# Optimization experiments

Measured on AMD Instinct MI355X. Metric: run time of the kernel, lower is better.

## Reference

```python
import jax, jax.numpy as jnp
import numpy as np

EPS = 1e-10
BETA = 1.0  # beta passed to VectorQuantizer in Encoder_conv


def _conv(x, w, b, stride, pad):
    # x: NCHW, w: OIHW
    y = jax.lax.conv_general_dilated(x, w, window_strides=stride, padding=pad,
                                     dimension_numbers=('NCHW', 'OIHW', 'NCHW'))
    if b is not None:
        y = y + b[None, :, None, None]
    return y


def _forward(x, w_in, b_in, w_h1, b_h1, w_h2, b_h2, w_h3, b_h3,
             r0_w1, r0_w2, r1_w1, r1_w2, emb):
    relu = jax.nn.relu
    h = relu(_conv(x, w_in, b_in, (2, 2), [(1, 1), (1, 1)]))      # [B,128,256,256]
    h = relu(_conv(h, w_h1, b_h1, (4, 4), [(2, 2), (2, 2)]))      # [B,256,64,64]
    h = relu(_conv(h, w_h2, b_h2, (4, 4), [(2, 2), (2, 2)]))      # [B,256,16,16]
    h = relu(_conv(h, w_h3, b_h3, (2, 2), [(1, 1), (1, 1)]))      # [B,256,8,8]
    # ResidualBlock with 2 Residual layers: relu->conv[1,3]->relu->conv[1,1], no bias
    for wa, wb in ((r0_w1, r0_w2), (r1_w1, r1_w2)):
        t = _conv(relu(h), wa, None, (1, 1), [(0, 0), (1, 1)])
        t = _conv(relu(t), wb, None, (1, 1), [(0, 0), (0, 0)])
        h = h + t
    h = relu(h)
    # VectorQuantizer
    lat = jnp.transpose(h, (0, 2, 3, 1))                          # [B,H,W,D]
    D = emb.shape[1]
    flat = lat.reshape(-1, D)                                     # [N,D]
    dist = (jnp.sum(flat * flat, axis=1, keepdims=True)
            + jnp.sum(emb * emb, axis=1)
            - 2.0 * flat @ emb.T)                                 # [N,K]
    idx = jnp.argmin(dist, axis=1)                                # [N]
    quant = emb[idx].reshape(lat.shape)                           # [B,H,W,D]
    sg = jax.lax.stop_gradient
    e_loss = jnp.mean((sg(quant) - lat) ** 2)
    q_loss = jnp.mean((quant - sg(lat)) ** 2)
    loss = q_loss + BETA * e_loss
    quant_st = lat + sg(quant - lat)                              # straight-through
    probs = jnp.mean(jax.nn.one_hot(idx, emb.shape[0], dtype=lat.dtype), axis=0)
    perplexity = jnp.exp(-jnp.sum(probs * jnp.log(probs + EPS)))
    return jnp.transpose(quant_st, (0, 3, 1, 2)), loss, perplexity


def setup_inputs() -> dict:
    key = jax.random.key(0)
    ks = jax.random.split(key, 14)
    C_in, C, K = 3, 256, 512
    s = 0.05
    f32 = jnp.float32
    return {
        'x':     jax.random.normal(ks[0], (8, C_in, 512, 512), f32),
        'w_in':  jax.random.normal(ks[1], (C // 2, C_in, 4, 4), f32) * s,
        'b_in':  jnp.zeros((C // 2,), f32),
        'w_h1':  jax.random.normal(ks[2], (C, C // 2, 7, 7), f32) * s,
        'b_h1':  jnp.zeros((C,), f32),
        'w_h2':  jax.random.normal(ks[3], (C, C, 7, 7), f32) * s,
        'b_h2':  jnp.zeros((C,), f32),
        'w_h3':  jax.random.normal(ks[4], (C, C, 3, 3), f32) * s,
        'b_h3':  jnp.zeros((C,), f32),
        'r0_w1': jax.random.normal(ks[5], (4 * C, C, 1, 3), f32) * s,
        'r0_w2': jax.random.normal(ks[6], (C, 4 * C, 1, 1), f32) * s,
        'r1_w1': jax.random.normal(ks[7], (4 * C, C, 1, 3), f32) * s,
        'r1_w2': jax.random.normal(ks[8], (C, 4 * C, 1, 1), f32) * s,
        'emb':   jax.random.uniform(ks[9], (K, C), f32, -1.0 / K, 1.0 / K),
    }


def reference(x, w_in, b_in, w_h1, b_h1, w_h2, b_h2, w_h3, b_h3,
              r0_w1, r0_w2, r1_w1, r1_w2, emb):
    return _forward(x, w_in, b_in, w_h1, b_h1, w_h2, b_h2, w_h3, b_h3,
                    r0_w1, r0_w2, r1_w1, r1_w2, emb)
```

## Files before the change

### kernel.cpp

```cpp
#include <hip/hip_runtime.h>
#include <hip/hip_bf16.h>

typedef __hip_bfloat16 bf16;
typedef __attribute__((ext_vector_type(4))) float f32x4;
typedef __attribute__((ext_vector_type(8))) short short8;

__device__ __forceinline__ float b2f(bf16 v) { return __bfloat162float(v); }
__device__ __forceinline__ ushort f2bu(float v)
{
    bf16 b = __float2bfloat16(v);
    return *(ushort*)&b;
}
__device__ __forceinline__ uint relu2(uint v)
{
    uint r = v;
    if (r & 0x8000u)     r &= 0xFFFF0000u;
    if (r & 0x80000000u) r &= 0x0000FFFFu;
    return r;
}
__device__ __forceinline__ uint packbf2(float a, float b)
{
    uint lo = f2bu(a), hi = f2bu(b);
    return lo | (hi << 16);
}

typedef const __attribute__((address_space(1))) unsigned int* as1_u32;
typedef __attribute__((address_space(3))) unsigned int* as3_u32;
__device__ __forceinline__ void gld16(const void* g, uint* l)
{
    __builtin_amdgcn_global_load_lds((as1_u32)g, (as3_u32)l, 16, 0, 0);
}

__global__ __launch_bounds__(256) void initw_k(
        const float* __restrict__ w_in, const float* __restrict__ w_h1,
        const float* __restrict__ w_h2, const float* __restrict__ w_h3,
        const float* __restrict__ r0w1, const float* __restrict__ r0w2,
        const float* __restrict__ r1w1, const float* __restrict__ r1w2,
        const float* __restrict__ emb,
        bf16* __restrict__ wp1, bf16* __restrict__ wpack2, bf16* __restrict__ wpack3,
        bf16* __restrict__ wp4, bf16* __restrict__ wpA0, bf16* __restrict__ wpA1,
        bf16* __restrict__ wpB0, bf16* __restrict__ wpB1,
        float* __restrict__ en, float* __restrict__ mse, int* __restrict__ hist,
        float* __restrict__ zpad)
{
    __shared__ ushort ls[12544];
    int b = blockIdx.x, t = threadIdx.x;

    if (b < 256) {
        const float* src = w_h1 + (size_t)b * 6272;
        for (int i = t; i < 6272; i += 256) ls[i] = f2bu(src[i]);
        __syncthreads();
        for (int e = t; e < 800; e += 256) {
            int tap = e >> 4, cib8 = e & 15;
            short8 v;
            #pragma unroll
            for (int cil = 0; cil < 8; ++cil)
                v[cil] = (tap < 49) ? (short)ls[(cib8 * 8 + cil) * 49 + tap] : (short)0;
            *(short8*)(wpack2 + ((size_t)(tap * 16 + cib8) * 256 + b) * 8) = v;
        }
        return;
    }
    if (b < 512) {
        int co = b - 256;
        const float* src = w_h2 + (size_t)co * 12544;
        for (int i = t; i < 12544; i += 256) ls[i] = f2bu(src[i]);
        __syncthreads();
        for (int e = t; e < 1600; e += 256) {
            int tap = e >> 5, cib8 = e & 31;
            short8 v;
            #pragma unroll
            for (int cil = 0; cil < 8; ++cil)
                v[cil] = (tap < 49) ? (short)ls[(cib8 * 8 + cil) * 49 + tap] : (short)0;
            *(short8*)(wpack3 + ((size_t)(tap * 32 + cib8) * 256 + co) * 8) = v;
        }
        return;
    }
    if (b < 768) {
        int co = b - 512;
        const float* src = w_h3 + (size_t)co * 2304;
        for (int i = t; i < 2304; i += 256) ls[i] = f2bu(src[i]);
        __syncthreads();
        for (int e = t; e < 288; e += 256) {
            int tap = e >> 5, cib8 = e & 31;
            short8 v;
            #pragma unroll
            for (int cil = 0; cil < 8; ++cil)
                v[cil] = (short)ls[(cib8 * 8 + cil) * 9 + tap];
            *(short8*)(wp4 + ((size_t)(tap * 32 + cib8) * 256 + co) * 8) = v;
        }
        return;
    }
    if (b < 2816) {
        int r = b - 768;
        int which = r >> 10;
        int co = r & 1023;
        const float* srcb = which ? r1w1 : r0w1;
        bf16* dstb = which ? wpA1 : wpA0;
        const float* src = srcb + (size_t)co * 768;
        for (int i = t; i < 768; i += 256) ls[i] = f2bu(src[i]);
        __syncthreads();
        if (t < 96) {
            int tap = t >> 5, cib8 = t & 31;
            short8 v;
            #pragma unroll
            for (int cil = 0; cil < 8; ++cil)
                v[cil] = (short)ls[(cib8 * 8 + cil) * 3 + tap];
            *(short8*)(dstb + ((size_t)(tap * 32 + cib8) * 1024 + co) * 8) = v;
        }
        return;
    }
    if (b < 3072) {
        int r = b - 2816;
        int which = r >> 7;
        const float* srcb = which ? r1w2 : r0w2;
        bf16* dstb = which ? wpB1 : wpB0;
        int c = (r & 127) * 256 + t;
        int cib8 = c >> 8, co = c & 255;
        const float* s = srcb + (size_t)co * 1024 + cib8 * 8;
        short8 v;
        #pragma unroll
        for (int cil = 0; cil < 8; ++cil) v[cil] = (short)f2bu(s[cil]);
        *(short8*)(dstb + (size_t)c * 8) = v;
        return;
    }
    if (b < 3104) {
        int i = (b - 3072) * 256 + t;
        int j = i & 7; int co = (i >> 3) & 127; int kb = i >> 10;
        int k = kb * 8 + j;
        wp1[i] = __float2bfloat16(k < 48 ? w_in[co * 48 + k] : 0.f);
        return;
    }
    if (b < 3106) {
        int row = (b - 3104) * 256 + t;
        const float4* e = (const float4*)(emb + (size_t)row * 256);
        float s = 0.f;
        for (int d4 = 0; d4 < 64; ++d4) {
            float4 v = e[d4];
            s += v.x * v.x + v.y * v.y + v.z * v.z + v.w * v.w;
        }
        en[row] = s;
        return;
    }
    if (t == 0) mse[0] = 0.f;
    for (int i = t; i < 512; i += 256) hist[i] = 0;
    if (t < 64) zpad[t] = 0.f;
}

__global__ __launch_bounds__(256) void conv1m_k(const float* __restrict__ x,
        const bf16* __restrict__ wp1, const float* __restrict__ bias,
        bf16* __restrict__ h1c)
{
    int bid = blockIdx.x;
    int pxt = bid & 511, img = bid >> 9;
    int tr = pxt >> 4, tc = pxt & 15;
    int oh0 = tr * 8, ow0 = tc * 16;
    const float* xi = x + (size_t)img * 786432;
    bf16* oT = h1c + (size_t)img * 8388608;

    int t = threadIdx.x;
    int wave = t >> 6, lane = t & 63;
    int quad = lane >> 4, l15 = lane & 15;

    __shared__ ushort xs[4 * 640];
    __shared__ ushort ot[128 * 136];

    int ihb = oh0 * 2 - 1, iwb = ow0 * 2 - 1;
    for (int i = t; i < 1836; i += 256) {
        int ci = i / 612; int r1 = i - ci * 612;
        int ihl = r1 / 34, iwl = r1 - ihl * 34;
        int ih = ihb + ihl, iw = iwb + iwl;
        float v = 0.f;
        if ((unsigned)ih < 512u && (unsigned)iw < 512u)
            v = xi[ci * 262144 + ih * 512 + iw];
        xs[ci * 640 + ihl * 35 + iwl] = f2bu(v);
    }
    for (int i = t; i < 640; i += 256) xs[3 * 640 + i] = 0;
    __syncthreads();

    f32x4 zero = {0.f, 0.f, 0.f, 0.f};
    f32x4 acc[8][2];
    #pragma unroll
    for (int m = 0; m < 8; ++m) { acc[m][0] = zero; acc[m][1] = zero; }

    int ci_b = quad >> 1;
    int kh0 = (quad & 1) * 2;
    int iwl0 = 2 * l15;

    #pragma unroll
    for (int ks = 0; ks < 2; ++ks) {
        union { short8 v; uint u[4]; } b[2];
        #pragma unroll
        for (int nt = 0; nt < 2; ++nt) {
            int py = wave * 2 + nt;
            int base = (ks * 2 + ci_b) * 640 + (2 * py + kh0) * 35 + iwl0;
            b[nt].u[0] = *(const uint*)&xs[base];
            b[nt].u[1] = *(const uint*)&xs[base + 2];
            b[nt].u[2] = *(const uint*)&xs[base + 35];
            b[nt].u[3] = *(const uint*)&xs[base + 37];
        }
        const bf16* abase = wp1 + ((size_t)(ks * 4 + quad) * 128 + l15) * 8;
        #pragma unroll
        for (int m = 0; m < 8; ++m) {
            short8 a = *(const short8*)(abase + m * 16 * 8);
            acc[m][0] = __builtin_amdgcn_mfma_f32_16x16x32_bf16(a, b[0].v, acc[m][0], 0, 0, 0);
            acc[m][1] = __builtin_amdgcn_mfma_f32_16x16x32_bf16(a, b[1].v, acc[m][1], 0, 0, 0);
        }
    }

    #pragma unroll
    for (int m = 0; m < 8; ++m) {
        int cobase = m * 16 + quad * 4;
        float b0 = bias[cobase], b1 = bias[cobase + 1];
        float b2 = bias[cobase + 2], b3 = bias[cobase + 3];
        #pragma unroll
        for (int nt = 0; nt < 2; ++nt) {
            int pxl = (wave * 2 + nt) * 16 + l15;
            uint w0 = packbf2(fmaxf(b0 + acc[m][nt][0], 0.f),
                              fmaxf(b1 + acc[m][nt][1], 0.f));
            uint w1 = packbf2(fmaxf(b2 + acc[m][nt][2], 0.f),
                              fmaxf(b3 + acc[m][nt][3], 0.f));
            *(uint*)&ot[pxl * 136 + cobase]     = w0;
            *(uint*)&ot[pxl * 136 + cobase + 2] = w1;
        }
    }
    __syncthreads();
    {
        int pxl = t >> 1, half = t & 1;
        int oh = oh0 + (pxl >> 4), ow = ow0 + (pxl & 15);
        size_t px = (size_t)(oh * 256 + ow);
        #pragma unroll
        for (int cb = 0; cb < 4; ++cb) {
            int c16 = half * 4 + cb;
            const uint4* src = (const uint4*)&ot[pxl * 136 + c16 * 16];
            uint4* dst = (uint4*)(oT + ((size_t)c16 * 65536 + px) * 16);
            dst[0] = src[0];
            dst[1] = src[1];
        }
    }
}

template <int IH, int OH, int CI, int SPLIT, int MODE>
__global__ __launch_bounds__(256, 2) void conv_mfma9_k(
        const bf16* __restrict__ inC, const bf16* __restrict__ wpack,
        const float* __restrict__ bias, float* __restrict__ outA,
        bf16* __restrict__ outT, const float* __restrict__ zpad)
{
    constexpr int TPD = OH / 8;
    constexpr int NT = TPD * TPD;
    constexpr int CPB = (CI / 16) / SPLIT;
    constexpr int CIB8 = CI / 8;
    constexpr int NPX = IH * IH;
    constexpr int SLOTS = 2496;

    int bid = blockIdx.x;
    int pxt = bid % NT;
    int rest = bid / NT;
    int img = rest & 7;
    int split = rest >> 3;
    int oh0 = (pxt / TPD) * 8, ow0 = (pxt % TPD) * 8;

    int t = threadIdx.x;
    int wave = t >> 6, lane = t & 63;
    int quad = lane >> 4, l15 = lane & 15;

    const bf16* inb = inC + (size_t)img * ((size_t)NPX * CI);

    __shared__ __align__(16) uint bufA[SLOTS * 4];
    __shared__ __align__(16) uint bufB[SLOTS * 4];

    f32x4 zero = {0.f, 0.f, 0.f, 0.f};
    f32x4 acc[4][4];
    #pragma unroll
    for (int a = 0; a < 4; ++a)
        #pragma unroll
        for (int b = 0; b < 4; ++b) acc[a][b] = zero;

    int ihb = oh0 * 4 - 2, iwb = ow0 * 4 - 2;
    int qxl = l15 & 7, pyl = l15 >> 3;
    int tap_par = quad >> 1, ci_half = quad & 1;

    int  srel[10];
    bool sval[10];
    #pragma unroll
    for (int it = 0; it < 10; ++it) {
        int sb = (it < 9) ? it * 256 + wave * 64 : 2304 + wave * 64;
        int p  = sb + lane;
        int pb = p << 4;
        int lb = pb ^ (((pb >> 7) & 7) << 4);
        int j  = lb >> 4;
        int pos = j >> 1, half = j & 1;
        int r = pos / 35, c = pos - r * 35;
        int ih = ihb + r, iw = iwb + c;
        sval[it] = (j < 2450) && ((unsigned)ih < (unsigned)IH)
                   && ((unsigned)iw < (unsigned)IH);
        srel[it] = (ih * IH + iw) * 16 + half * 8;
    }

    auto stage = [&](int ch, uint* dst) {
        const bf16* cbp = inb + (size_t)ch * NPX * 16;
        #pragma unroll
        for (int it = 0; it < 10; ++it) {
            if (it == 9 && wave >= 3) continue;
            int sb = (it < 9) ? it * 256 + wave * 64 : 2304 + wave * 64;
            const void* src = sval[it] ? (const void*)(cbp + srel[it])
                                       : (const void*)zpad;
            gld16(src, dst + sb * 4);
        }
    };

    int rbase = pyl * 4480 + qxl * 128 + ci_half * 16;
    int d1  = tap_par * 32;
    int d29 = tap_par * 928;

    auto compute = [&](int ch, const uint* cbuf) {
        const bf16* ab = wpack
            + ((size_t)(ch * 2 + ci_half) * 256 + wave * 64 + l15) * 8
            + (size_t)tap_par * (CIB8 * 2048);
        __builtin_amdgcn_s_setprio(1);
        short8 aC[4], bC[4], aN[4], bN[4];
        {
            #pragma unroll
            for (int ct = 0; ct < 4; ++ct)
                aC[ct] = *(const short8*)(ab + ct * 128);
            int lbb = rbase + d1;
            #pragma unroll
            for (int pt = 0; pt < 4; ++pt) {
                int lb = lbb + pt * 8960;
                int pb = lb ^ (((lb >> 7) & 7) << 4);
                bC[pt] = *(const short8*)((const char*)cbuf + pb);
            }
        }
        #pragma unroll
        for (int tp = 0; tp < 25; ++tp) {
            if (tp < 24) {
                const int tn  = tp + 1;
                const int kh0 = (2 * tn) / 7, kw0 = (2 * tn) % 7;
                const int cE  = (kh0 * 35 + kw0) * 32;
                int dsel = (tn == 24) ? 0 : ((kw0 == 6) ? d29 : d1);
                int lbb  = rbase + cE + dsel;
                const bf16* at = ab + (size_t)(2 * tn) * (CIB8 * 2048);
                #pragma unroll
                for (int ct = 0; ct < 4; ++ct)
                    aN[ct] = *(const short8*)(at + ct * 128);
                #pragma unroll
                for (int pt = 0; pt < 4; ++pt) {
                    int lb = lbb + pt * 8960;
                    int pb = lb ^ (((lb >> 7) & 7) << 4);
                    bN[pt] = *(const short8*)((const char*)cbuf + pb);
                }
            }
            #pragma unroll
            for (int pt = 0; pt < 4; ++pt)
                #pragma unroll
                for (int ct = 0; ct < 4; ++ct)
                    acc[ct][pt] = __builtin_amdgcn_mfma_f32_16x16x32_bf16(
                        aC[ct], bC[pt], acc[ct][pt], 0, 0, 0);
            if (tp < 24) {
                #pragma unroll
                for (int i = 0; i < 4; ++i) { aC[i] = aN[i]; bC[i] = bN[i]; }
            }
        }
        __builtin_amdgcn_s_setprio(0);
    };

    if constexpr (CPB == 1) {
        stage(split, bufA);
        __syncthreads();
        compute(split, bufA);
    } else {
        stage(split * CPB, bufA);
        __syncthreads();
        for (int cc2 = 0; cc2 < CPB; cc2 += 2) {
            stage(split * CPB + cc2 + 1, bufB);
            compute(split * CPB + cc2, bufA);
            __syncthreads();
            if (cc2 + 2 < CPB) stage(split * CPB + cc2 + 2, bufA);
            compute(split * CPB + cc2 + 1, bufB);
            __syncthreads();
        }
    }

    #pragma unroll
    for (int ct = 0; ct < 4; ++ct) {
        int cobase = wave * 64 + ct * 16 + quad * 4;
        #pragma unroll
        for (int pt = 0; pt < 4; ++pt) {
            int px = pt * 16 + l15;
            int oh = oh0 + (px >> 3), ow = ow0 + (px & 7);
            int pxg = oh * OH + ow;
            if (MODE == 3) {
                #pragma unroll
                for (int r = 0; r < 4; ++r) {
                    int co = cobase + r;
                    outA[(size_t)split * ((size_t)8 * OH * OH * 256)
                         + (size_t)img * (OH * OH * 256)
                         + (size_t)co * (OH * OH) + pxg] = acc[ct][pt][r];
                }
            } else {
                float o0 = fmaxf(bias[cobase]     + acc[ct][pt][0], 0.f);
                float o1 = fmaxf(bias[cobase + 1] + acc[ct][pt][1], 0.f);
                float o2 = fmaxf(bias[cobase + 2] + acc[ct][pt][2], 0.f);
                float o3 = fmaxf(bias[cobase + 3] + acc[ct][pt][3], 0.f);
                uint2 w;
                w.x = packbf2(o0, o1);
                w.y = packbf2(o2, o3);
                size_t base = (size_t)img * (size_t)(OH * OH * 256);
                *(uint2*)(outT + base
                          + ((size_t)(wave * 4 + ct) * (OH * OH) + pxg) * 16
                          + quad * 4) = w;
            }
        }
    }
}

__global__ void combine3_k(const float* __restrict__ p3, const float* __restrict__ bias,
                           bf16* __restrict__ h3T)
{
    int idx = blockIdx.x * 256 + threadIdx.x;
    int px = idx & 255;
    int co = (idx >> 8) & 255;
    int img = idx >> 16;
    float v = bias[co];
    #pragma unroll
    for (int s = 0; s < 8; ++s) v += p3[(size_t)s * 524288 + idx];
    v = fmaxf(v, 0.f);
    h3T[((size_t)img * 256 + px) * 256 + co] = __float2bfloat16(v);
}

__global__ __launch_bounds__(256) void conv4m_k(const bf16* __restrict__ h3T,
        const bf16* __restrict__ wp4, const float* __restrict__ bias,
        bf16* __restrict__ h4T)
{
    int bid = blockIdx.x;
    int img = bid >> 2, cog = bid & 3;
    int t = threadIdx.x;
    int wave = t >> 6, lane = t & 63;
    int quad = lane >> 4, l15 = lane & 15;

    __shared__ uint pt[16 * 325];

    for (int i = t; i < 16 * 325; i += 256) pt[i] = 0;

    f32x4 zero = {0.f, 0.f, 0.f, 0.f};
    f32x4 acc[4];
    #pragma unroll
    for (int b = 0; b < 4; ++b) acc[b] = zero;

    const bf16* inb = h3T + (size_t)img * 65536;

    for (int ch = 0; ch < 8; ++ch) {
        __syncthreads();
        for (int e = t; e < 4096; e += 256) {
            int cp = e & 15, px = e >> 4;
            int py = px >> 4, qx = px & 15;
            uint v = *(const uint*)(inb + (size_t)px * 256 + ch * 32 + cp * 2);
            pt[cp * 325 + (py + 1) * 18 + qx + 1] = v;
        }
        __syncthreads();

        for (int tap = 0; tap < 9; ++tap) {
            int kh = tap / 3, kw = tap - kh * 3;
            const bf16* abase = wp4 + ((size_t)((tap * 32 + ch * 4 + quad) * 256)
                                       + cog * 64 + wave * 16 + l15) * 8;
            short8 a = *(const short8*)abase;
            #pragma unroll
            for (int pq = 0; pq < 4; ++pq) {
                int pyo = 2 * pq + (l15 >> 3);
                int ipos = (2 * pyo + kh) * 18 + 2 * (l15 & 7) + kw;
                union { short8 v; uint u[4]; } b;
                b.u[0] = pt[(quad * 4 + 0) * 325 + ipos];
                b.u[1] = pt[(quad * 4 + 1) * 325 + ipos];
                b.u[2] = pt[(quad * 4 + 2) * 325 + ipos];
                b.u[3] = pt[(quad * 4 + 3) * 325 + ipos];
                acc[pq] = __builtin_amdgcn_mfma_f32_16x16x32_bf16(
                    a, b.v, acc[pq], 0, 0, 0);
            }
        }
    }

    int cobase = cog * 64 + wave * 16 + quad * 4;
    #pragma unroll
    for (int pq = 0; pq < 4; ++pq) {
        int px = pq * 16 + l15;
        #pragma unroll
        for (int r = 0; r < 4; ++r) {
            int co = cobase + r;
            float v = fmaxf(bias[co] + acc[pq][r], 0.f);
            h4T[((size_t)img * 64 + px) * 256 + co] = __float2bfloat16(v);
        }
    }
}

__global__ __launch_bounds__(256) void resam_k(const bf16* __restrict__ hT,
        const bf16* __restrict__ wpA, bf16* __restrict__ t1T)
{
    int bid = blockIdx.x;
    int img = bid >> 4, g = bid & 15;
    int t = threadIdx.x;
    int wave = t >> 6, lane = t & 63;
    int quad = lane >> 4, l15 = lane & 15;

    __shared__ uint ph[128 * 81];

    for (int i = t; i < 128 * 81; i += 256) ph[i] = 0;
    __syncthreads();
    const bf16* inb = hT + (size_t)img * 16384;
    for (int e = t; e < 8192; e += 256) {
        int cp = e & 127, px = e >> 7;
        uint v = relu2(*(const uint*)(inb + (size_t)px * 256 + cp * 2));
        ph[cp * 81 + (px >> 3) * 10 + (px & 7) + 1] = v;
    }
    __syncthreads();

    f32x4 zero = {0.f, 0.f, 0.f, 0.f};
    f32x4 acc[4];
    #pragma unroll
    for (int b = 0; b < 4; ++b) acc[b] = zero;

    for (int ch = 0; ch < 8; ++ch) {
        for (int tap = 0; tap < 3; ++tap) {
            const bf16* abase = wpA + ((size_t)(tap * 32 + ch * 4 + quad) * 1024
                                       + g * 64 + wave * 16 + l15) * 8;
            short8 a = *(const short8*)abase;
            #pragma unroll
            for (int pq = 0; pq < 4; ++pq) {
                int py = 2 * pq + (l15 >> 3);
                int pos = py * 10 + (l15 & 7) + tap;
                union { short8 v; uint u[4]; } b;
                b.u[0] = ph[(ch * 16 + quad * 4 + 0) * 81 + pos];
                b.u[1] = ph[(ch * 16 + quad * 4 + 1) * 81 + pos];
                b.u[2] = ph[(ch * 16 + quad * 4 + 2) * 81 + pos];
                b.u[3] = ph[(ch * 16 + quad * 4 + 3) * 81 + pos];
                acc[pq] = __builtin_amdgcn_mfma_f32_16x16x32_bf16(
                    a, b.v, acc[pq], 0, 0, 0);
            }
        }
    }

    int cobase = g * 64 + wave * 16 + quad * 4;
    #pragma unroll
    for (int pq = 0; pq < 4; ++pq) {
        int px = pq * 16 + l15;
        #pragma unroll
        for (int r = 0; r < 4; ++r)
            t1T[((size_t)img * 64 + px) * 1024 + cobase + r]
                = __float2bfloat16(acc[pq][r]);
    }
}

__global__ __launch_bounds__(256) void resbm_k(const bf16* __restrict__ holdT,
        const bf16* __restrict__ t1T, const bf16* __restrict__ wpB,
        bf16* __restrict__ hnewT)
{
    int bid = blockIdx.x;
    int img = bid >> 3, cog = (bid >> 1) & 3, ph = bid & 1;
    int t = threadIdx.x;
    int wave = t >> 6, lane = t & 63;
    int quad = lane >> 4, l15 = lane & 15;

    __shared__ uint pb[256 * 33];

    f32x4 zero = {0.f, 0.f, 0.f, 0.f};
    f32x4 acc[2];
    acc[0] = zero; acc[1] = zero;

    const bf16* inb = t1T + (size_t)img * 65536 + (size_t)ph * 32 * 1024;

    for (int s = 0; s < 2; ++s) {
        __syncthreads();
        for (int e = t; e < 8192; e += 256) {
            int cp = e & 255, pxl = e >> 8;
            uint v = relu2(*(const uint*)(inb + (size_t)pxl * 1024 + s * 512 + cp * 2));
            pb[cp * 33 + pxl] = v;
        }
        __syncthreads();

        for (int chl = 0; chl < 16; ++chl) {
            int ch = s * 16 + chl;
            const bf16* abase = wpB + ((size_t)(ch * 4 + quad) * 256
                                       + cog * 64 + wave * 16 + l15) * 8;
            short8 a = *(const short8*)abase;
            #pragma unroll
            for (int pq = 0; pq < 2; ++pq) {
                int pxl = pq * 16 + l15;
                union { short8 v; uint u[4]; } b;
                b.u[0] = pb[(chl * 16 + quad * 4 + 0) * 33 + pxl];
                b.u[1] = pb[(chl * 16 + quad * 4 + 1) * 33 + pxl];
                b.u[2] = pb[(chl * 16 + quad * 4 + 2) * 33 + pxl];
                b.u[3] = pb[(chl * 16 + quad * 4 + 3) * 33 + pxl];
                acc[pq] = __builtin_amdgcn_mfma_f32_16x16x32_bf16(
                    a, b.v, acc[pq], 0, 0, 0);
            }
        }
    }

    int cobase = cog * 64 + wave * 16 + quad * 4;
    #pragma unroll
    for (int pq = 0; pq < 2; ++pq) {
        int px = ph * 32 + pq * 16 + l15;
        #pragma unroll
        for (int r = 0; r < 4; ++r) {
            int co = cobase + r;
            size_t o = ((size_t)img * 64 + px) * 256 + co;
            float v = b2f(holdT[o]) + acc[pq][r];
            hnewT[o] = __float2bfloat16(v);
        }
    }
}

__global__ __launch_bounds__(256) void vq_k(const bf16* __restrict__ h6T,
        const float* __restrict__ emb, const float* __restrict__ en,
        float* __restrict__ out, float* __restrict__ mse_acc, int* __restrict__ hist)
{
    int row0 = blockIdx.x * 2;
    int t = threadIdx.x;
    int wave = t >> 6, lane = t & 63;
    __shared__ float lat[2][256];
    __shared__ float swd[4][2];
    __shared__ int   swi[4][2];
    __shared__ int   fidx[2];
    __shared__ float smse[4];

    for (int e = t; e < 512; e += 256) {
        int r = e >> 8, c = e & 255;
        lat[r][c] = fmaxf(b2f(h6T[(size_t)(row0 + r) * 256 + c]), 0.f);
    }
    __syncthreads();

    float a0[2] = {0.f, 0.f}, a1[2] = {0.f, 0.f};
    const float4* e0 = (const float4*)(emb + (size_t)t * 256);
    const float4* e1 = (const float4*)(emb + (size_t)(t + 256) * 256);
    for (int d4 = 0; d4 < 64; ++d4) {
        float4 v0 = e0[d4], v1 = e1[d4];
        #pragma unroll
        for (int r = 0; r < 2; ++r) {
            float l0 = lat[r][d4 * 4], l1 = lat[r][d4 * 4 + 1];
            float l2 = lat[r][d4 * 4 + 2], l3 = lat[r][d4 * 4 + 3];
            a0[r] += l0 * v0.x + l1 * v0.y + l2 * v0.z + l3 * v0.w;
            a1[r] += l0 * v1.x + l1 * v1.y + l2 * v1.z + l3 * v1.w;
        }
    }
    float en0 = en[t], en1 = en[t + 256];
    float bd[2]; int bi[2];
    #pragma unroll
    for (int r = 0; r < 2; ++r) {
        float d0 = en0 - 2.f * a0[r], d1v = en1 - 2.f * a1[r];
        bd[r] = d0; bi[r] = t;
        if (d1v < bd[r]) { bd[r] = d1v; bi[r] = t + 256; }
    }
    #pragma unroll
    for (int s = 1; s < 64; s <<= 1) {
        #pragma unroll
        for (int r = 0; r < 2; ++r) {
            float od = __shfl_xor(bd[r], s);
            int   oi = __shfl_xor(bi[r], s);
            if (od < bd[r] || (od == bd[r] && oi < bi[r])) { bd[r] = od; bi[r] = oi; }
        }
    }
    if (lane == 0) {
        #pragma unroll
        for (int r = 0; r < 2; ++r) { swd[wave][r] = bd[r]; swi[wave][r] = bi[r]; }
    }
    __syncthreads();
    if (t < 2) {
        float best = swd[0][t]; int bidx = swi[0][t];
        for (int w = 1; w < 4; ++w) {
            float od = swd[w][t]; int oi = swi[w][t];
            if (od < best || (od == best && oi < bidx)) { best = od; bidx = oi; }
        }
        fidx[t] = bidx;
    }
    __syncthreads();

    float msel = 0.f;
    #pragma unroll
    for (int r = 0; r < 2; ++r) {
        int row = row0 + r;
        int b = row >> 6, y = (row >> 3) & 7, xx = row & 7;
        float q = emb[(size_t)fidx[r] * 256 + t];
        out[((size_t)(b * 256 + t) * 8 + y) * 8 + xx] = q;
        float diff = q - lat[r][t];
        msel += diff * diff;
    }
    #pragma unroll
    for (int s = 1; s < 64; s <<= 1) msel += __shfl_xor(msel, s);
    if (lane == 0) smse[wave] = msel;
    __syncthreads();
    if (t == 0) atomicAdd(mse_acc, smse[0] + smse[1] + smse[2] + smse[3]);
    if (t < 2) atomicAdd(&hist[fidx[t]], 1);
}

__global__ void final_k(const float* __restrict__ mse_acc, const int* __restrict__ hist,
                        float* __restrict__ out)
{
    __shared__ float sh[512];
    int t = threadIdx.x;
    float p = (float)hist[t] / 512.f;
    sh[t] = p * logf(p + 1e-10f);
    __syncthreads();
    for (int s = 256; s > 0; s >>= 1) {
        if (t < s) sh[t] += sh[t + s];
        __syncthreads();
    }
    if (t == 0) {
        float loss = 2.f * mse_acc[0] / (512.f * 256.f);
        float perp = expf(-sh[0]);
        out[131072] = loss;
        out[131073] = perp;
    }
}

extern "C" void kernel_launch(void* const* d_in, const int* in_sizes, int n_in,
                              void* d_out, int out_size, void* d_ws, size_t ws_size,
                              hipStream_t stream)
{
    const float* x    = (const float*)d_in[0];
    const float* w_in = (const float*)d_in[1];
    const float* b_in = (const float*)d_in[2];
    const float* w_h1 = (const float*)d_in[3];
    const float* b_h1 = (const float*)d_in[4];
    const float* w_h2 = (const float*)d_in[5];
    const float* b_h2 = (const float*)d_in[6];
    const float* w_h3 = (const float*)d_in[7];
    const float* b_h3 = (const float*)d_in[8];
    const float* r0w1 = (const float*)d_in[9];
    const float* r0w2 = (const float*)d_in[10];
    const float* r1w1 = (const float*)d_in[11];
    const float* r1w2 = (const float*)d_in[12];
    const float* emb  = (const float*)d_in[13];
    float* out = (float*)d_out;

    char* ws = (char*)d_ws;
    size_t off = 0;
    auto alloc = [&](size_t bytes) -> void* {
        void* p = ws + off;
        off += (bytes + 255) & ~(size_t)255;
        return p;
    };

    float* en  = (float*)alloc(512 * 4);
    float* mse = (float*)alloc(256);
    int*  hist = (int*)alloc(512 * 4);
    float* zpad = (float*)alloc(256);
    float* p3  = (float*)alloc(4194304ull * 4);
    bf16* h3T  = (bf16*)alloc(524288ull * 2);
    bf16* h4T  = (bf16*)alloc(131072ull * 2);
    bf16* t1T  = (bf16*)alloc(524288ull * 2);
    bf16* h5T  = (bf16*)alloc(131072ull * 2);
    bf16* h6T  = (bf16*)alloc(131072ull * 2);
    bf16* wp1  = (bf16*)alloc(8192ull * 2);
    bf16* wpack2 = (bf16*)alloc(1638400ull * 2);
    bf16* wpack3 = (bf16*)alloc(3276800ull * 2);
    bf16* wp4  = (bf16*)alloc(589824ull * 2);
    bf16* wpA0 = (bf16*)alloc(786432ull * 2);
    bf16* wpA1 = (bf16*)alloc(786432ull * 2);
    bf16* wpB0 = (bf16*)alloc(262144ull * 2);
    bf16* wpB1 = (bf16*)alloc(262144ull * 2);
    bf16* h2c  = (bf16*)alloc(8388608ull * 2);
    size_t base_end = off;

    const size_t H1F_B = 8388608ull * 8 * 2;
    size_t needT1 = base_end + H1F_B + 4096;
    bf16* h1c;
    int tier;
    if (ws_size >= needT1) {
        h1c = (bf16*)alloc(H1F_B);
        tier = 1;
    } else {
        h1c = (bf16*)alloc(8388608ull * 2);
        tier = 2;
    }

    initw_k<<<3107, 256, 0, stream>>>(w_in, w_h1, w_h2, w_h3, r0w1, r0w2, r1w1, r1w2,
        emb, wp1, wpack2, wpack3, wp4, wpA0, wpA1, wpB0, wpB1, en, mse, hist, zpad);

    if (tier == 1) {
        conv1m_k<<<4096, 256, 0, stream>>>(x, wp1, b_in, h1c);
        conv_mfma9_k<256, 64, 128, 1, 0><<<512, 256, 0, stream>>>(
            h1c, wpack2, b_h1, nullptr, h2c, zpad);
    } else {
        for (int n = 0; n < 8; ++n) {
            conv1m_k<<<512, 256, 0, stream>>>(x + (size_t)n * 786432, wp1, b_in, h1c);
            conv_mfma9_k<256, 64, 128, 1, 0><<<64, 256, 0, stream>>>(
                h1c, wpack2, b_h1, nullptr, h2c + (size_t)n * 1048576, zpad);
        }
    }

    conv_mfma9_k<64, 16, 256, 8, 3><<<256, 256, 0, stream>>>(
        h2c, wpack3, nullptr, p3, nullptr, zpad);
    combine3_k<<<2048, 256, 0, stream>>>(p3, b_h2, h3T);

    conv4m_k<<<32, 256, 0, stream>>>(h3T, wp4, b_h3, h4T);
    resam_k<<<128, 256, 0, stream>>>(h4T, wpA0, t1T);
    resbm_k<<<64, 256, 0, stream>>>(h4T, t1T, wpB0, h5T);
    resam_k<<<128, 256, 0, stream>>>(h5T, wpA1, t1T);
    resbm_k<<<64, 256, 0, stream>>>(h5T, t1T, wpB1, h6T);

    vq_k<<<256, 256, 0, stream>>>(h6T, emb, en, out, mse, hist);
    final_k<<<1, 512, 0, stream>>>(mse, hist, out);
}
```

Measured before the change: 444.3 us.

## Pair images per block in conv2, split conv4 rows, fuse final reduction into VQ

```diff
diff --git a/kernel.cpp b/kernel.cpp
--- a/kernel.cpp
+++ b/kernel.cpp
@@ -41,7 +41,7 @@
         bf16* __restrict__ wp4, bf16* __restrict__ wpA0, bf16* __restrict__ wpA1,
         bf16* __restrict__ wpB0, bf16* __restrict__ wpB1,
         float* __restrict__ en, float* __restrict__ mse, int* __restrict__ hist,
-        float* __restrict__ zpad)
+        float* __restrict__ zpad, int* __restrict__ done)
 {
     __shared__ ushort ls[12544];
     int b = blockIdx.x, t = threadIdx.x;
@@ -144,6 +144,7 @@
     if (t == 0) mse[0] = 0.f;
     for (int i = t; i < 512; i += 256) hist[i] = 0;
     if (t < 64) zpad[t] = 0.f;
+    if (t == 64) done[0] = 0;
 }
 
 __global__ __launch_bounds__(256) void conv1m_k(const float* __restrict__ x,
@@ -239,8 +240,8 @@
     }
 }
 
-template <int IH, int OH, int CI, int SPLIT, int MODE>
-__global__ __launch_bounds__(256, 2) void conv_mfma9_k(
+template <int IH, int OH, int CI, int SPLIT, int MODE, int PAIR>
+__global__ __launch_bounds__(PAIR ? 512 : 256, 2) void conv_mfma12_k(
         const bf16* __restrict__ inC, const bf16* __restrict__ wpack,
         const float* __restrict__ bias, float* __restrict__ outA,
         bf16* __restrict__ outT, const float* __restrict__ zpad)
@@ -255,18 +256,27 @@
     int bid = blockIdx.x;
     int pxt = bid % NT;
     int rest = bid / NT;
-    int img = rest & 7;
-    int split = rest >> 3;
-    int oh0 = (pxt / TPD) * 8, ow0 = (pxt % TPD) * 8;
-
     int t = threadIdx.x;
     int wave = t >> 6, lane = t & 63;
     int quad = lane >> 4, l15 = lane & 15;
 
+    int wl, img, split;
+    if (PAIR) {
+        wl = wave & 3;
+        split = rest >> 2;
+        img = (rest & 3) * 2 + (wave >> 2);
+    } else {
+        wl = wave;
+        img = rest & 7;
+        split = rest >> 3;
+    }
+    int oh0 = (pxt / TPD) * 8, ow0 = (pxt % TPD) * 8;
+
     const bf16* inb = inC + (size_t)img * ((size_t)NPX * CI);
 
-    __shared__ __align__(16) uint bufA[SLOTS * 4];
-    __shared__ __align__(16) uint bufB[SLOTS * 4];
+    __shared__ __align__(16) uint bufs[PAIR ? 4 : 2][SLOTS * 4];
+    uint* bufA = bufs[PAIR ? ((wave >> 2) * 2) : 0];
+    uint* bufB = bufs[(PAIR ? ((wave >> 2) * 2) : 0) + 1];
 
     f32x4 zero = {0.f, 0.f, 0.f, 0.f};
     f32x4 acc[4][4];
@@ -283,7 +293,7 @@
     bool sval[10];
     #pragma unroll
     for (int it = 0; it < 10; ++it) {
-        int sb = (it < 9) ? it * 256 + wave * 64 : 2304 + wave * 64;
+        int sb = (it < 9) ? it * 256 + wl * 64 : 2304 + wl * 64;
         int p  = sb + lane;
         int pb = p << 4;
         int lb = pb ^ (((pb >> 7) & 7) << 4);
@@ -300,8 +310,8 @@
         const bf16* cbp = inb + (size_t)ch * NPX * 16;
         #pragma unroll
         for (int it = 0; it < 10; ++it) {
-            if (it == 9 && wave >= 3) continue;
-            int sb = (it < 9) ? it * 256 + wave * 64 : 2304 + wave * 64;
+            if (it == 9 && wl >= 3) continue;
+            int sb = (it < 9) ? it * 256 + wl * 64 : 2304 + wl * 64;
             const void* src = sval[it] ? (const void*)(cbp + srel[it])
                                        : (const void*)zpad;
             gld16(src, dst + sb * 4);
@@ -314,7 +324,7 @@
 
     auto compute = [&](int ch, const uint* cbuf) {
         const bf16* ab = wpack
-            + ((size_t)(ch * 2 + ci_half) * 256 + wave * 64 + l15) * 8
+            + ((size_t)(ch * 2 + ci_half) * 256 + wl * 64 + l15) * 8
             + (size_t)tap_par * (CIB8 * 2048);
         __builtin_amdgcn_s_setprio(1);
         short8 aC[4], bC[4], aN[4], bN[4];
@@ -382,7 +392,7 @@
 
     #pragma unroll
     for (int ct = 0; ct < 4; ++ct) {
-        int cobase = wave * 64 + ct * 16 + quad * 4;
+        int cobase = wl * 64 + ct * 16 + quad * 4;
         #pragma unroll
         for (int pt = 0; pt < 4; ++pt) {
             int px = pt * 16 + l15;
@@ -406,7 +416,7 @@
                 w.y = packbf2(o2, o3);
                 size_t base = (size_t)img * (size_t)(OH * OH * 256);
                 *(uint2*)(outT + base
-                          + ((size_t)(wave * 4 + ct) * (OH * OH) + pxg) * 16
+                          + ((size_t)(wl * 4 + ct) * (OH * OH) + pxg) * 16
                           + quad * 4) = w;
             }
         }
@@ -432,29 +442,32 @@
         bf16* __restrict__ h4T)
 {
     int bid = blockIdx.x;
-    int img = bid >> 2, cog = bid & 3;
+    int img = bid >> 3, cog = (bid >> 1) & 3, ph = bid & 1;
     int t = threadIdx.x;
     int wave = t >> 6, lane = t & 63;
     int quad = lane >> 4, l15 = lane & 15;
 
-    __shared__ uint pt[16 * 325];
-
-    for (int i = t; i < 16 * 325; i += 256) pt[i] = 0;
+    __shared__ uint pt[16 * 163];
+
+    for (int i = t; i < 16 * 163; i += 256) pt[i] = 0;
 
     f32x4 zero = {0.f, 0.f, 0.f, 0.f};
-    f32x4 acc[4];
-    #pragma unroll
-    for (int b = 0; b < 4; ++b) acc[b] = zero;
+    f32x4 acc[2];
+    acc[0] = zero; acc[1] = zero;
 
     const bf16* inb = h3T + (size_t)img * 65536;
 
     for (int ch = 0; ch < 8; ++ch) {
         __syncthreads();
-        for (int e = t; e < 4096; e += 256) {
-            int cp = e & 15, px = e >> 4;
-            int py = px >> 4, qx = px & 15;
-            uint v = *(const uint*)(inb + (size_t)px * 256 + ch * 32 + cp * 2);
-            pt[cp * 325 + (py + 1) * 18 + qx + 1] = v;
+        for (int e = t; e < 2304; e += 256) {
+            int cp = e & 15, rem = e >> 4;
+            int sr = rem >> 4, qx = rem & 15;
+            int gr = ph * 8 + sr - 1;
+            if ((unsigned)gr < 16u) {
+                uint v = *(const uint*)(inb + (size_t)(gr * 16 + qx) * 256
+                                        + ch * 32 + cp * 2);
+                pt[cp * 163 + sr * 18 + qx + 1] = v;
+            }
         }
         __syncthreads();
 
@@ -464,14 +477,14 @@
                                        + cog * 64 + wave * 16 + l15) * 8;
             short8 a = *(const short8*)abase;
             #pragma unroll
-            for (int pq = 0; pq < 4; ++pq) {
+            for (int pq = 0; pq < 2; ++pq) {
                 int pyo = 2 * pq + (l15 >> 3);
                 int ipos = (2 * pyo + kh) * 18 + 2 * (l15 & 7) + kw;
                 union { short8 v; uint u[4]; } b;
-                b.u[0] = pt[(quad * 4 + 0) * 325 + ipos];
-                b.u[1] = pt[(quad * 4 + 1) * 325 + ipos];
-                b.u[2] = pt[(quad * 4 + 2) * 325 + ipos];
-                b.u[3] = pt[(quad * 4 + 3) * 325 + ipos];
+                b.u[0] = pt[(quad * 4 + 0) * 163 + ipos];
+                b.u[1] = pt[(quad * 4 + 1) * 163 + ipos];
+                b.u[2] = pt[(quad * 4 + 2) * 163 + ipos];
+                b.u[3] = pt[(quad * 4 + 3) * 163 + ipos];
                 acc[pq] = __builtin_amdgcn_mfma_f32_16x16x32_bf16(
                     a, b.v, acc[pq], 0, 0, 0);
             }
@@ -480,8 +493,8 @@
 
     int cobase = cog * 64 + wave * 16 + quad * 4;
     #pragma unroll
-    for (int pq = 0; pq < 4; ++pq) {
-        int px = pq * 16 + l15;
+    for (int pq = 0; pq < 2; ++pq) {
+        int px = ph * 32 + pq * 16 + l15;
         #pragma unroll
         for (int r = 0; r < 4; ++r) {
             int co = cobase + r;
@@ -610,7 +623,8 @@
 
 __global__ __launch_bounds__(256) void vq_k(const bf16* __restrict__ h6T,
         const float* __restrict__ emb, const float* __restrict__ en,
-        float* __restrict__ out, float* __restrict__ mse_acc, int* __restrict__ hist)
+        float* __restrict__ out, float* __restrict__ mse_acc, int* __restrict__ hist,
+        int* __restrict__ done)
 {
     int row0 = blockIdx.x * 2;
     int t = threadIdx.x;
@@ -620,6 +634,7 @@
     __shared__ int   swi[4][2];
     __shared__ int   fidx[2];
     __shared__ float smse[4];
+    __shared__ int   lastf;
 
     for (int e = t; e < 512; e += 256) {
         int r = e >> 8, c = e & 255;
@@ -688,25 +703,32 @@
     __syncthreads();
     if (t == 0) atomicAdd(mse_acc, smse[0] + smse[1] + smse[2] + smse[3]);
     if (t < 2) atomicAdd(&hist[fidx[t]], 1);
-}
-
-__global__ void final_k(const float* __restrict__ mse_acc, const int* __restrict__ hist,
-                        float* __restrict__ out)
-{
-    __shared__ float sh[512];
-    int t = threadIdx.x;
-    float p = (float)hist[t] / 512.f;
-    sh[t] = p * logf(p + 1e-10f);
-    __syncthreads();
-    for (int s = 256; s > 0; s >>= 1) {
-        if (t < s) sh[t] += sh[t + s];
-        __syncthreads();
-    }
+    __syncthreads();
+
     if (t == 0) {
-        float loss = 2.f * mse_acc[0] / (512.f * 256.f);
-        float perp = expf(-sh[0]);
-        out[131072] = loss;
-        out[131073] = perp;
+        __threadfence();
+        int d = atomicAdd(done, 1);
+        lastf = (d == 255);
+    }
+    __syncthreads();
+    if (lastf) {
+        __threadfence();
+        float* sh = &lat[0][0];
+        int h0 = __hip_atomic_load(&hist[t],       __ATOMIC_RELAXED, __HIP_MEMORY_SCOPE_AGENT);
+        int h1 = __hip_atomic_load(&hist[t + 256], __ATOMIC_RELAXED, __HIP_MEMORY_SCOPE_AGENT);
+        float p0 = (float)h0 / 512.f, p1 = (float)h1 / 512.f;
+        __syncthreads();
+        sh[t] = p0 * logf(p0 + 1e-10f) + p1 * logf(p1 + 1e-10f);
+        __syncthreads();
+        for (int s = 128; s > 0; s >>= 1) {
+            if (t < s) sh[t] += sh[t + s];
+            __syncthreads();
+        }
+        if (t == 0) {
+            float m = __hip_atomic_load(mse_acc, __ATOMIC_RELAXED, __HIP_MEMORY_SCOPE_AGENT);
+            out[131072] = 2.f * m / (512.f * 256.f);
+            out[131073] = expf(-sh[0]);
+        }
     }
 }
 
@@ -742,6 +764,7 @@
     float* mse = (float*)alloc(256);
     int*  hist = (int*)alloc(512 * 4);
     float* zpad = (float*)alloc(256);
+    int*  done = (int*)alloc(256);
     float* p3  = (float*)alloc(4194304ull * 4);
     bf16* h3T  = (bf16*)alloc(524288ull * 2);
     bf16* h4T  = (bf16*)alloc(131072ull * 2);
@@ -772,30 +795,29 @@
     }
 
     initw_k<<<3107, 256, 0, stream>>>(w_in, w_h1, w_h2, w_h3, r0w1, r0w2, r1w1, r1w2,
-        emb, wp1, wpack2, wpack3, wp4, wpA0, wpA1, wpB0, wpB1, en, mse, hist, zpad);
+        emb, wp1, wpack2, wpack3, wp4, wpA0, wpA1, wpB0, wpB1, en, mse, hist, zpad, done);
 
     if (tier == 1) {
         conv1m_k<<<4096, 256, 0, stream>>>(x, wp1, b_in, h1c);
-        conv_mfma9_k<256, 64, 128, 1, 0><<<512, 256, 0, stream>>>(
+        conv_mfma12_k<256, 64, 128, 1, 0, 1><<<256, 512, 0, stream>>>(
             h1c, wpack2, b_h1, nullptr, h2c, zpad);
     } else {
         for (int n = 0; n < 8; ++n) {
             conv1m_k<<<512, 256, 0, stream>>>(x + (size_t)n * 786432, wp1, b_in, h1c);
-            conv_mfma9_k<256, 64, 128, 1, 0><<<64, 256, 0, stream>>>(
+            conv_mfma12_k<256, 64, 128, 1, 0, 0><<<64, 256, 0, stream>>>(
                 h1c, wpack2, b_h1, nullptr, h2c + (size_t)n * 1048576, zpad);
         }
     }
 
-    conv_mfma9_k<64, 16, 256, 8, 3><<<256, 256, 0, stream>>>(
+    conv_mfma12_k<64, 16, 256, 8, 3, 0><<<256, 256, 0, stream>>>(
         h2c, wpack3, nullptr, p3, nullptr, zpad);
     combine3_k<<<2048, 256, 0, stream>>>(p3, b_h2, h3T);
 
-    conv4m_k<<<32, 256, 0, stream>>>(h3T, wp4, b_h3, h4T);
+    conv4m_k<<<64, 256, 0, stream>>>(h3T, wp4, b_h3, h4T);
     resam_k<<<128, 256, 0, stream>>>(h4T, wpA0, t1T);
     resbm_k<<<64, 256, 0, stream>>>(h4T, t1T, wpB0, h5T);
     resam_k<<<128, 256, 0, stream>>>(h5T, wpA1, t1T);
     resbm_k<<<64, 256, 0, stream>>>(h5T, t1T, wpB1, h6T);
 
-    vq_k<<<256, 256, 0, stream>>>(h6T, emb, en, out, mse, hist);
-    final_k<<<1, 512, 0, stream>>>(mse, hist, out);
-}
+    vq_k<<<256, 256, 0, stream>>>(h6T, emb, en, out, mse, hist, done);
+}
```

Result: slower. 467.5 us (+5.2%).
